# Kernel tuning notes

Measured on AMD Instinct MI355X. Metric: run time of the kernel, lower is better.

The kernel has to match this reference:

```python
import jax, jax.numpy as jnp
import numpy as np

A = 32      # num_agents (nodes per batch element)
B = 256     # batch size
T = 5       # temporal_window_size
H, C = 4, 64  # attention heads, hidden_dim per head
D = H * C   # feature_dim = 256
NEG_SLOPE = 0.2
LATENT = 128
NBS = 64    # num_belief_states
FIN = NBS + 16  # node_feat_dim = num_belief_states + action_dim


def _xavier(k, shape):
    std = (2.0 / (shape[0] + shape[-1])) ** 0.5
    return std * jax.random.normal(k, shape, dtype=jnp.float32)


def setup_inputs() -> dict:
    key = jax.random.key(0)
    ks = jax.random.split(key, 24)
    N = B * A
    # fully-connected directed graph (no self loops) inside each batch block
    ii, jj = np.meshgrid(np.arange(A), np.arange(A), indexing='ij')
    m = ii != jj
    off = (np.arange(B) * A)[:, None]
    src = (off + ii[m][None, :]).ravel()
    dst = (off + jj[m][None, :]).ravel()
    edge_index = jnp.asarray(np.stack([src, dst]), dtype=jnp.int32)  # [2, E]
    return dict(
        x_seq=jax.random.normal(ks[0], (T, N, FIN), dtype=jnp.float32),
        edge_index=edge_index,
        W1=_xavier(ks[1], (D, FIN)),
        att_src1=0.1 * jax.random.normal(ks[2], (H, C), dtype=jnp.float32),
        att_dst1=0.1 * jax.random.normal(ks[3], (H, C), dtype=jnp.float32),
        b1=jnp.zeros((D,), jnp.float32),
        W2=_xavier(ks[4], (D, D)),
        att_src2=0.1 * jax.random.normal(ks[5], (H, C), dtype=jnp.float32),
        att_dst2=0.1 * jax.random.normal(ks[6], (H, C), dtype=jnp.float32),
        b2=jnp.zeros((D,), jnp.float32),
        in_proj_w=_xavier(ks[7], (3 * D, D)),
        in_proj_b=jnp.zeros((3 * D,), jnp.float32),
        out_proj_w=_xavier(ks[8], (D, D)),
        out_proj_b=jnp.zeros((D,), jnp.float32),
        w_mean=_xavier(ks[9], (LATENT, D)),
        b_mean=jnp.zeros((LATENT,), jnp.float32),
        w_logvar=_xavier(ks[10], (LATENT, D)),
        b_logvar=jnp.zeros((LATENT,), jnp.float32),
        w_belief=_xavier(ks[11], (NBS, D)),
        b_belief=jnp.zeros((NBS,), jnp.float32),
    )


def _gat(x, src, dst, W, a_src, a_dst, bias, N):
    """PyG-style GATConv (concat heads, self loops already in src/dst, eval mode)."""
    h = (x @ W.T).reshape(N, H, C)                         # [N,H,C]
    e = (h * a_src).sum(-1)[src] + (h * a_dst).sum(-1)[dst]  # [E,H]
    e = jax.nn.leaky_relu(e, NEG_SLOPE)
    mx = jax.ops.segment_max(e, dst, num_segments=N)       # segment softmax over incoming edges
    ex = jnp.exp(e - mx[dst])
    denom = jax.ops.segment_sum(ex, dst, num_segments=N)
    alpha = ex / denom[dst]                                # [E,H]
    out = jax.ops.segment_sum(h[src] * alpha[:, :, None], dst, num_segments=N)
    return out.reshape(N, H * C) + bias


def reference(x_seq, edge_index, W1, att_src1, att_dst1, b1, W2, att_src2, att_dst2, b2,
              in_proj_w, in_proj_b, out_proj_w, out_proj_b,
              w_mean, b_mean, w_logvar, b_logvar, w_belief, b_belief):
    N = x_seq.shape[1]
    loops = jnp.arange(N, dtype=edge_index.dtype)          # GATConv adds self loops
    src = jnp.concatenate([edge_index[0], loops])
    dst = jnp.concatenate([edge_index[1], loops])
    ego = jnp.arange(0, N, A)                              # ego node of each batch element

    def step(_, x):
        hh = jax.nn.relu(_gat(x, src, dst, W1, att_src1, att_dst1, b1, N))
        hh = jax.nn.relu(_gat(hh, src, dst, W2, att_src2, att_dst2, b2, N))
        return None, hh[ego]                               # [B, D]

    _, outs = jax.lax.scan(step, None, x_seq)              # [T, B, D]
    seq = jnp.transpose(outs, (1, 0, 2))                   # [B, T, D]

    # nn.MultiheadAttention(batch_first=True), float additive mask of 1s (j<=i) / 0s (j>i)
    qkv = seq @ in_proj_w.T + in_proj_b
    q, k, v = jnp.split(qkv, 3, axis=-1)
    split = lambda t: t.reshape(B, T, H, D // H).transpose(0, 2, 1, 3)  # [B,H,T,dh]
    q, k, v = split(q), split(k), split(v)
    mask = (jnp.arange(T)[:, None] >= jnp.arange(T)[None, :]).astype(seq.dtype)
    scale = 1.0 / jnp.sqrt(jnp.asarray(D // H, seq.dtype))
    scores = jnp.einsum('bhqd,bhkd->bhqk', q, k) * scale + mask
    attn = jax.nn.softmax(scores, axis=-1)
    ctx = jnp.einsum('bhqk,bhkd->bhqd', attn, v).transpose(0, 2, 1, 3).reshape(B, T, D)
    attn_out = ctx @ out_proj_w.T + out_proj_b
    feat = attn_out[:, -1]                                 # [B, D]

    mean = feat @ w_mean.T + b_mean
    logvar = feat @ w_logvar.T + b_logvar
    belief = jax.nn.softmax(feat @ w_belief.T + b_belief, axis=-1)
    return mean, logvar, belief
```

## Files before the change

### kernel.cpp

```cpp
#include <hip/hip_runtime.h>

typedef _Float16 f16;
typedef __attribute__((ext_vector_type(2))) _Float16 f16x2;
typedef __attribute__((ext_vector_type(4))) _Float16 f16x4;
typedef __attribute__((ext_vector_type(8))) _Float16 f16x8;
typedef __attribute__((ext_vector_type(4))) float    f32x4;

#define NA 32
#define NB 256
#define NT 5
#define ND 256
#define NFIN 80
#define NLAT 128
#define NBEL 64
#define NEG 0.2f

#define W1K 96
#define XSTR 104
#define H1TSTR 40
#define HH1STR 264
#define ALSTR 40

#define OFF_XS  0
#define OFF_ALP 6656
#define OFF_HH1 0
#define OFF_H1T 16896
#define OFF_SD  37376
#define SMEM_SZ 38400

#define MFMA16(a,b,c) __builtin_amdgcn_mfma_f32_16x16x32_f16(a, b, c, 0, 0, 0)

#define WS_SEQ   0
#define WS_QKV   655360
#define WS_CTX   2621440
#define WS_W1F   2752512
#define WS_W2F   2801664
#define WS_IPW   2932736
#define WS_OPW   3325952
#define WS_HDW   3457024
#define WS_WSD1  3620864
#define WS_WSD2  3623936

__global__ void convert_w(const float* __restrict__ W1, const float* __restrict__ W2,
                          const float* __restrict__ ipw, const float* __restrict__ opw,
                          const float* __restrict__ wm, const float* __restrict__ wl,
                          const float* __restrict__ wb,
                          const float* __restrict__ as1, const float* __restrict__ ad1,
                          const float* __restrict__ as2, const float* __restrict__ ad2,
                          f16* __restrict__ W1f, f16* __restrict__ W2f,
                          f16* __restrict__ ipwf, f16* __restrict__ opwf,
                          f16* __restrict__ hdwf,
                          f16* __restrict__ wsd1f, f16* __restrict__ wsd2f)
{
    const int i = blockIdx.x * 256 + threadIdx.x;
    if (i < 24576) {
        const int r = i / W1K, c = i - r * W1K;
        W1f[i] = (c < NFIN) ? (f16)W1[r * NFIN + c] : (f16)0.f;
    } else if (i < 90112) {
        const int j = i - 24576; W2f[j] = (f16)W2[j];
    } else if (i < 286720) {
        const int j = i - 90112; ipwf[j] = (f16)ipw[j];
    } else if (i < 352256) {
        const int j = i - 286720; opwf[j] = (f16)opw[j];
    } else if (i < 434176) {
        const int j = i - 352256;
        hdwf[j] = (f16)(j < 32768 ? wm[j] : (j < 65536 ? wl[j - 32768] : wb[j - 65536]));
    } else if (i < 435712) {
        const int j = i - 434176;
        const int o = j / 96, f = j - o * 96;
        float v = 0.f;
        if (o < 8 && f < NFIN) {
            const int h = o & 3;
            const float* av = (o < 4) ? as1 : ad1;
            for (int cc = 0; cc < 64; ++cc)
                v = fmaf(av[h * 64 + cc], W1[(h * 64 + cc) * NFIN + f], v);
        }
        wsd1f[j] = (f16)v;
    } else if (i < 439808) {
        const int j = i - 435712;
        const int o = j >> 8, k = j & 255;
        float v = 0.f;
        if (o < 8) {
            const int h = o & 3;
            const float* av = (o < 4) ? as2 : ad2;
            for (int cc = 0; cc < 64; ++cc)
                v = fmaf(av[h * 64 + cc], W2[(h * 64 + cc) * ND + k], v);
        }
        wsd2f[j] = (f16)v;
    }
}

__global__ __launch_bounds__(256, 4)
void gnn_kernel(const float* __restrict__ x_seq,
                const f16*  __restrict__ W1f,  const f16* __restrict__ wsd1f,
                const float* __restrict__ b1,
                const f16*  __restrict__ W2f,  const f16* __restrict__ wsd2f,
                const float* __restrict__ b2,
                f16* __restrict__ seqf)
{
    __shared__ __align__(16) unsigned char smem[SMEM_SZ];
    f16*  Xs  = (f16*)(smem + OFF_XS);
    f16*  hh1 = (f16*)(smem + OFF_HH1);
    f16*  alp = (f16*)(smem + OFF_ALP);
    f16*  h1T = (f16*)(smem + OFF_H1T);
    float* sA = (float*)(smem + OFF_SD);
    float* dA = sA + 128;

    const int blk  = blockIdx.x;
    const int b    = blk / NT;
    const int t    = blk % NT;
    const int tid  = threadIdx.x;
    const int wv   = tid >> 6;
    const int lane = tid & 63;
    const int c    = lane & 15;
    const int g    = lane >> 4;
    const int n0   = wv * 64;

    const float* xg = x_seq + ((size_t)t * (NB * NA) + (size_t)b * NA) * NFIN;
    for (int idx = tid; idx < 640; idx += 256) {
        const int r = idx / 20, c4 = idx - r * 20;
        const float4 v = ((const float4*)xg)[idx];
        f16x4 h; h.x = (f16)v.x; h.y = (f16)v.y; h.z = (f16)v.z; h.w = (f16)v.w;
        *(f16x4*)(Xs + r * XSTR + c4 * 4) = h;
    }
    if (tid < 128) {
        const int r = tid >> 2, cc = tid & 3;
        f16x4 z; z.x = z.y = z.z = z.w = (f16)0.f;
        *(f16x4*)(Xs + r * XSTR + 80 + cc * 4) = z;
    }
    __syncthreads();

    f32x4 acc1[2][4]; f32x4 accS[2];
#pragma unroll
    for (int m = 0; m < 2; ++m) {
        accS[m] = (f32x4)0.f;
#pragma unroll
        for (int tn = 0; tn < 4; ++tn) acc1[m][tn] = (f32x4)0.f;
    }
#pragma unroll
    for (int kt = 0; kt < 3; ++kt) {
        const int k0 = kt * 32 + 8 * g;
        f16x8 a0 = *(const f16x8*)(Xs + c * XSTR + k0);
        f16x8 a1 = *(const f16x8*)(Xs + (16 + c) * XSTR + k0);
        f16x8 bs = *(const f16x8*)(wsd1f + c * W1K + k0);
        accS[0] = MFMA16(a0, bs, accS[0]);
        accS[1] = MFMA16(a1, bs, accS[1]);
#pragma unroll
        for (int tn = 0; tn < 4; ++tn) {
            f16x8 bw = *(const f16x8*)(W1f + (size_t)(n0 + 16 * tn + c) * W1K + k0);
            acc1[0][tn] = MFMA16(a0, bw, acc1[0][tn]);
            acc1[1][tn] = MFMA16(a1, bw, acc1[1][tn]);
        }
    }

    if (c == wv) {
#pragma unroll
        for (int m = 0; m < 2; ++m)
#pragma unroll
            for (int r = 0; r < 4; ++r)
                sA[wv * 32 + 16 * m + 4 * g + r] = accS[m][r];
    } else if (c == wv + 4) {
#pragma unroll
        for (int m = 0; m < 2; ++m)
#pragma unroll
            for (int r = 0; r < 4; ++r)
                dA[wv * 32 + 16 * m + 4 * g + r] = accS[m][r];
    }

#pragma unroll
    for (int m = 0; m < 2; ++m)
#pragma unroll
        for (int tn = 0; tn < 4; ++tn) {
            f16x4 h;
            h.x = (f16)acc1[m][tn][0]; h.y = (f16)acc1[m][tn][1];
            h.z = (f16)acc1[m][tn][2]; h.w = (f16)acc1[m][tn][3];
            *(f16x4*)(h1T + (n0 + 16 * tn + c) * H1TSTR + 16 * m + 4 * g) = h;
        }

    {
        const int j = lane & 31;
        const int half = lane >> 5;
        const float dd = dA[wv * 32 + j];
        const float* sbase = sA + wv * 32 + 16 * half;
        float e[16]; float mx = -1e30f;
#pragma unroll
        for (int i = 0; i < 16; ++i) {
            float v = sbase[i] + dd;
            v = (v >= 0.f) ? v : NEG * v;
            e[i] = v; mx = fmaxf(mx, v);
        }
        mx = fmaxf(mx, __shfl_xor(mx, 32, 64));
        float den = 0.f;
#pragma unroll
        for (int i = 0; i < 16; ++i) { float p = __expf(e[i] - mx); e[i] = p; den += p; }
        den += __shfl_xor(den, 32, 64);
        const float rr = 1.f / den;
        f16* arow = alp + (wv * 32 + j) * ALSTR + 16 * half;
#pragma unroll
        for (int i2 = 0; i2 < 8; ++i2) {
            f16x2 p2; p2.x = (f16)(e[2 * i2] * rr); p2.y = (f16)(e[2 * i2 + 1] * rr);
            *(f16x2*)(arow + 2 * i2) = p2;
        }
    }

    f32x4 agg[2][4];
#pragma unroll
    for (int m = 0; m < 2; ++m)
#pragma unroll
        for (int tn = 0; tn < 4; ++tn) agg[m][tn] = (f32x4)0.f;
    {
        f16x8 aal0 = *(const f16x8*)(alp + (wv * 32 + c) * ALSTR + 8 * g);
        f16x8 aal1 = *(const f16x8*)(alp + (wv * 32 + 16 + c) * ALSTR + 8 * g);
#pragma unroll
        for (int tn = 0; tn < 4; ++tn) {
            f16x8 bh = *(const f16x8*)(h1T + (n0 + 16 * tn + c) * H1TSTR + 8 * g);
            agg[0][tn] = MFMA16(aal0, bh, agg[0][tn]);
            agg[1][tn] = MFMA16(aal1, bh, agg[1][tn]);
        }
    }

    __syncthreads();

    {
        float b1v[4];
#pragma unroll
        for (int tn = 0; tn < 4; ++tn) b1v[tn] = b1[n0 + 16 * tn + c];
#pragma unroll
        for (int m = 0; m < 2; ++m)
#pragma unroll
            for (int tn = 0; tn < 4; ++tn)
#pragma unroll
                for (int r = 0; r < 4; ++r) {
                    float val = fmaxf(agg[m][tn][r] + b1v[tn], 0.f);
                    hh1[(16 * m + 4 * g + r) * HH1STR + n0 + 16 * tn + c] = (f16)val;
                }
    }
    __syncthreads();

    f32x4 acc2[2][4]; f32x4 accS2[2];
#pragma unroll
    for (int m = 0; m < 2; ++m) {
        accS2[m] = (f32x4)0.f;
#pragma unroll
        for (int tn = 0; tn < 4; ++tn) acc2[m][tn] = (f32x4)0.f;
    }
#pragma unroll
    for (int kt = 0; kt < 8; ++kt) {
        const int k0 = kt * 32 + 8 * g;
        f16x8 a0 = *(const f16x8*)(hh1 + c * HH1STR + k0);
        f16x8 a1 = *(const f16x8*)(hh1 + (16 + c) * HH1STR + k0);
        f16x8 bs = *(const f16x8*)(wsd2f + c * ND + k0);
        accS2[0] = MFMA16(a0, bs, accS2[0]);
        accS2[1] = MFMA16(a1, bs, accS2[1]);
#pragma unroll
        for (int tn = 0; tn < 4; ++tn) {
            f16x8 bw = *(const f16x8*)(W2f + (size_t)(n0 + 16 * tn + c) * ND + k0);
            acc2[0][tn] = MFMA16(a0, bw, acc2[0][tn]);
            acc2[1][tn] = MFMA16(a1, bw, acc2[1][tn]);
        }
    }

    if (c == wv) {
#pragma unroll
        for (int m = 0; m < 2; ++m)
#pragma unroll
            for (int r = 0; r < 4; ++r)
                sA[wv * 32 + 16 * m + 4 * g + r] = accS2[m][r];
    }
    if (c == wv + 4 && g == 0) dA[wv * 32] = accS2[0][0];

    const float d20 = dA[wv * 32];

    {
        float mx = -1e30f;
#pragma unroll
        for (int i = 0; i < 32; ++i) {
            float v = sA[wv * 32 + i] + d20;
            v = (v >= 0.f) ? v : NEG * v;
            mx = fmaxf(mx, v);
        }
        float den = 0.f;
#pragma unroll
        for (int i = 0; i < 32; ++i) {
            float v = sA[wv * 32 + i] + d20;
            v = (v >= 0.f) ? v : NEG * v;
            den += __expf(v - mx);
        }
        float ev[2][4];
#pragma unroll
        for (int m = 0; m < 2; ++m)
#pragma unroll
            for (int r = 0; r < 4; ++r) {
                float v = sA[wv * 32 + 16 * m + 4 * g + r] + d20;
                v = (v >= 0.f) ? v : NEG * v;
                ev[m][r] = __expf(v - mx);
            }
        float b2v[4];
#pragma unroll
        for (int tn = 0; tn < 4; ++tn) b2v[tn] = b2[n0 + 16 * tn + c];
        const float rden = 1.f / den;
        f16* sq = seqf + ((size_t)b * NT + t) * ND;
#pragma unroll
        for (int tn = 0; tn < 4; ++tn) {
            float o = 0.f;
#pragma unroll
            for (int m = 0; m < 2; ++m)
#pragma unroll
                for (int r = 0; r < 4; ++r) o = fmaf(ev[m][r], acc2[m][tn][r], o);
            o += __shfl_xor(o, 16, 64);
            o += __shfl_xor(o, 32, 64);
            if (g == 0) sq[n0 + 16 * tn + c] = (f16)fmaxf(o * rden + b2v[tn], 0.f);
        }
    }
}

#define QASTR 264
__global__ __launch_bounds__(256, 4)
void qkv_kernel(const f16* __restrict__ seqf, const f16* __restrict__ ipwf,
                const float* __restrict__ ipb, f16* __restrict__ qkv)
{
    __shared__ __align__(16) f16 As[64 * QASTR];

    const int bx  = blockIdx.x;
    const int m0  = (bx % 20) * 64;
    const int n0  = (bx / 20) * 128;
    const int tid = threadIdx.x;
    const int wv  = tid >> 6;
    const int lane = tid & 63;
    const int c   = lane & 15;
    const int g   = lane >> 4;
    const int mb  = (wv >> 1) * 32;
    const int nb  = n0 + (wv & 1) * 64;

    for (int idx = tid; idx < 2048; idx += 256) {
        const int r = idx >> 5, c8 = idx & 31;
        *(f16x8*)(As + r * QASTR + c8 * 8) =
            *(const f16x8*)(seqf + (size_t)(m0 + r) * ND + c8 * 8);
    }
    __syncthreads();

    f32x4 acc[2][4];
#pragma unroll
    for (int m = 0; m < 2; ++m)
#pragma unroll
        for (int tn = 0; tn < 4; ++tn) acc[m][tn] = (f32x4)0.f;

#pragma unroll
    for (int kt = 0; kt < 8; ++kt) {
        const int k0 = kt * 32 + 8 * g;
        f16x8 a0 = *(const f16x8*)(As + (mb + c) * QASTR + k0);
        f16x8 a1 = *(const f16x8*)(As + (mb + 16 + c) * QASTR + k0);
#pragma unroll
        for (int tn = 0; tn < 4; ++tn) {
            f16x8 bw = *(const f16x8*)(ipwf + (size_t)(nb + 16 * tn + c) * ND + k0);
            acc[0][tn] = MFMA16(a0, bw, acc[0][tn]);
            acc[1][tn] = MFMA16(a1, bw, acc[1][tn]);
        }
    }

    float bias[4];
#pragma unroll
    for (int tn = 0; tn < 4; ++tn) bias[tn] = ipb[nb + 16 * tn + c];
#pragma unroll
    for (int m = 0; m < 2; ++m)
#pragma unroll
        for (int tn = 0; tn < 4; ++tn)
#pragma unroll
            for (int r = 0; r < 4; ++r) {
                const int row = m0 + mb + 16 * m + 4 * g + r;
                qkv[(size_t)row * 768 + nb + 16 * tn + c] =
                    (f16)(acc[m][tn][r] + bias[tn]);
            }
}

__global__ __launch_bounds__(256, 4)
void attn_kernel(const f16* __restrict__ qkv, f16* __restrict__ ctx)
{
    const int b    = blockIdx.x;
    const int wv   = threadIdx.x >> 6;
    const int lane = threadIdx.x & 63;
    const int ch   = wv * 64 + lane;

    const float q = (float)qkv[(size_t)(b * 5 + 4) * 768 + ch];
    float kv[NT], vv[NT];
#pragma unroll
    for (int t = 0; t < NT; ++t) {
        kv[t] = (float)qkv[(size_t)(b * 5 + t) * 768 + 256 + ch];
        vv[t] = (float)qkv[(size_t)(b * 5 + t) * 768 + 512 + ch];
    }
    float sc[NT];
#pragma unroll
    for (int t = 0; t < NT; ++t) {
        float p = q * kv[t];
#pragma unroll
        for (int off = 32; off > 0; off >>= 1) p += __shfl_xor(p, off, 64);
        sc[t] = p * 0.125f;
    }
    float m = sc[0];
#pragma unroll
    for (int t = 1; t < NT; ++t) m = fmaxf(m, sc[t]);
    float den = 0.f, o = 0.f;
#pragma unroll
    for (int t = 0; t < NT; ++t) {
        float p = __expf(sc[t] - m);
        den += p;
        o = fmaf(p, vv[t], o);
    }
    ctx[(size_t)b * ND + ch] = (f16)(o / den);
}

#define FASTR 264
__global__ __launch_bounds__(256, 2)
void final_kernel(const f16* __restrict__ ctx,
                  const f16* __restrict__ opwf, const float* __restrict__ opb,
                  const f16* __restrict__ hdwf,
                  const float* __restrict__ bm, const float* __restrict__ blv,
                  const float* __restrict__ bb,
                  float* __restrict__ out)
{
    __shared__ __align__(16) f16 As[32 * FASTR];
    __shared__ __align__(16) f16 Fs[32 * FASTR];
    __shared__ __align__(16) float Bs[32 * 68];

    const int m0   = blockIdx.x * 32;
    const int tid  = threadIdx.x;
    const int wv   = tid >> 6;
    const int lane = tid & 63;
    const int c    = lane & 15;
    const int g    = lane >> 4;

    for (int idx = tid; idx < 1024; idx += 256) {
        const int r = idx >> 5, c8 = idx & 31;
        *(f16x8*)(As + r * FASTR + c8 * 8) =
            *(const f16x8*)(ctx + (size_t)(m0 + r) * ND + c8 * 8);
    }
    __syncthreads();

    {
        f32x4 acc[2][4];
#pragma unroll
        for (int m = 0; m < 2; ++m)
#pragma unroll
            for (int tn = 0; tn < 4; ++tn) acc[m][tn] = (f32x4)0.f;
#pragma unroll
        for (int kt = 0; kt < 8; ++kt) {
            const int k0 = kt * 32 + 8 * g;
            f16x8 a0 = *(const f16x8*)(As + c * FASTR + k0);
            f16x8 a1 = *(const f16x8*)(As + (16 + c) * FASTR + k0);
#pragma unroll
            for (int tn = 0; tn < 4; ++tn) {
                f16x8 bw = *(const f16x8*)(opwf + (size_t)(wv * 64 + 16 * tn + c) * ND + k0);
                acc[0][tn] = MFMA16(a0, bw, acc[0][tn]);
                acc[1][tn] = MFMA16(a1, bw, acc[1][tn]);
            }
        }
        float bias[4];
#pragma unroll
        for (int tn = 0; tn < 4; ++tn) bias[tn] = opb[wv * 64 + 16 * tn + c];
#pragma unroll
        for (int m = 0; m < 2; ++m)
#pragma unroll
            for (int tn = 0; tn < 4; ++tn)
#pragma unroll
                for (int r = 0; r < 4; ++r)
                    Fs[(16 * m + 4 * g + r) * FASTR + wv * 64 + 16 * tn + c] =
                        (f16)(acc[m][tn][r] + bias[tn]);
    }
    __syncthreads();

    {
        f32x4 acc[2][5];
#pragma unroll
        for (int m = 0; m < 2; ++m)
#pragma unroll
            for (int fi = 0; fi < 5; ++fi) acc[m][fi] = (f32x4)0.f;
#pragma unroll
        for (int kt = 0; kt < 8; ++kt) {
            const int k0 = kt * 32 + 8 * g;
            f16x8 a0 = *(const f16x8*)(Fs + c * FASTR + k0);
            f16x8 a1 = *(const f16x8*)(Fs + (16 + c) * FASTR + k0);
#pragma unroll
            for (int fi = 0; fi < 5; ++fi) {
                const int nf = 5 * wv + fi;
                f16x8 bw = *(const f16x8*)(hdwf + (size_t)(16 * nf + c) * ND + k0);
                acc[0][fi] = MFMA16(a0, bw, acc[0][fi]);
                acc[1][fi] = MFMA16(a1, bw, acc[1][fi]);
            }
        }
#pragma unroll
        for (int fi = 0; fi < 5; ++fi) {
            const int ocol = 16 * (5 * wv + fi) + c;
            float bias;
            if (ocol < 128)       bias = bm[ocol];
            else if (ocol < 256)  bias = blv[ocol - 128];
            else                  bias = bb[ocol - 256];
#pragma unroll
            for (int m = 0; m < 2; ++m)
#pragma unroll
                for (int r = 0; r < 4; ++r) {
                    const int row = 16 * m + 4 * g + r;
                    const float v = acc[m][fi][r] + bias;
                    if (ocol < 128)
                        out[(size_t)(m0 + row) * NLAT + ocol] = v;
                    else if (ocol < 256)
                        out[(size_t)NB * NLAT + (size_t)(m0 + row) * NLAT + (ocol - 128)] = v;
                    else
                        Bs[row * 68 + (ocol - 256)] = v;
                }
        }
    }
    __syncthreads();

    for (int rr = 0; rr < 8; ++rr) {
        const int row = wv * 8 + rr;
        float x = Bs[row * 68 + lane];
        float mm = x;
#pragma unroll
        for (int off = 32; off > 0; off >>= 1) mm = fmaxf(mm, __shfl_xor(mm, off, 64));
        float p = __expf(x - mm);
        float dd = p;
#pragma unroll
        for (int off = 32; off > 0; off >>= 1) dd += __shfl_xor(dd, off, 64);
        out[(size_t)2 * NB * NLAT + (size_t)(m0 + row) * NBEL + lane] = p / dd;
    }
}

extern "C" void kernel_launch(void* const* d_in, const int* in_sizes, int n_in,
                              void* d_out, int out_size, void* d_ws, size_t ws_size,
                              hipStream_t stream)
{
    (void)in_sizes; (void)n_in; (void)out_size; (void)ws_size;
    const float* x_seq = (const float*)d_in[0];
    const float* W1  = (const float*)d_in[2];
    const float* as1 = (const float*)d_in[3];
    const float* ad1 = (const float*)d_in[4];
    const float* b1  = (const float*)d_in[5];
    const float* W2  = (const float*)d_in[6];
    const float* as2 = (const float*)d_in[7];
    const float* ad2 = (const float*)d_in[8];
    const float* b2  = (const float*)d_in[9];
    const float* ipw = (const float*)d_in[10];
    const float* ipb = (const float*)d_in[11];
    const float* opw = (const float*)d_in[12];
    const float* opb = (const float*)d_in[13];
    const float* wm  = (const float*)d_in[14];
    const float* bm  = (const float*)d_in[15];
    const float* wl  = (const float*)d_in[16];
    const float* bl  = (const float*)d_in[17];
    const float* wb  = (const float*)d_in[18];
    const float* bb  = (const float*)d_in[19];

    char* ws = (char*)d_ws;
    f16* seqf  = (f16*)(ws + WS_SEQ);
    f16* qkv   = (f16*)(ws + WS_QKV);
    f16* ctx   = (f16*)(ws + WS_CTX);
    f16* W1f   = (f16*)(ws + WS_W1F);
    f16* W2f   = (f16*)(ws + WS_W2F);
    f16* ipwf  = (f16*)(ws + WS_IPW);
    f16* opwf  = (f16*)(ws + WS_OPW);
    f16* hdwf  = (f16*)(ws + WS_HDW);
    f16* wsd1f = (f16*)(ws + WS_WSD1);
    f16* wsd2f = (f16*)(ws + WS_WSD2);
    float* out = (float*)d_out;

    hipLaunchKernelGGL(convert_w, dim3(1718), dim3(256), 0, stream,
                       W1, W2, ipw, opw, wm, wl, wb, as1, ad1, as2, ad2,
                       W1f, W2f, ipwf, opwf, hdwf, wsd1f, wsd2f);
    hipLaunchKernelGGL(gnn_kernel, dim3(NB * NT), dim3(256), 0, stream,
                       x_seq, W1f, wsd1f, b1, W2f, wsd2f, b2, seqf);
    hipLaunchKernelGGL(qkv_kernel, dim3(120), dim3(256), 0, stream,
                       seqf, ipwf, ipb, qkv);
    hipLaunchKernelGGL(attn_kernel, dim3(NB), dim3(256), 0, stream, qkv, ctx);
    hipLaunchKernelGGL(final_kernel, dim3(8), dim3(256), 0, stream,
                       ctx, opwf, opb, hdwf, bm, bl, bb, out);
}
```

Measured before the change: 71.33 us.

## Software-prefetch global weight fragments in MFMA loops and transpose aggregation output

The GEMM k-loops in the GNN and QKV kernels now double-buffer their global weight fragments in registers, loading the next k-slice before issuing the MFMAs on the current one. This hides global/L2 latency behind MFMA work. The attention-aggregation MFMA swaps its operands to produce a transposed tile, so the bias+ReLU writeback can use vectorized float4 bias loads and f16x4 shared-memory stores. Launch bounds drop from 4 to 3 blocks per CU to leave room for the extra live registers, which may reduce occupancy.

```diff
diff --git a/kernel.cpp b/kernel.cpp
--- a/kernel.cpp
+++ b/kernel.cpp
@@ -90,7 +90,7 @@
     }
 }
 
-__global__ __launch_bounds__(256, 4)
+__global__ __launch_bounds__(256, 3)
 void gnn_kernel(const float* __restrict__ x_seq,
                 const f16*  __restrict__ W1f,  const f16* __restrict__ wsd1f,
                 const float* __restrict__ b1,
@@ -137,19 +137,35 @@
 #pragma unroll
         for (int tn = 0; tn < 4; ++tn) acc1[m][tn] = (f32x4)0.f;
     }
-#pragma unroll
-    for (int kt = 0; kt < 3; ++kt) {
-        const int k0 = kt * 32 + 8 * g;
-        f16x8 a0 = *(const f16x8*)(Xs + c * XSTR + k0);
-        f16x8 a1 = *(const f16x8*)(Xs + (16 + c) * XSTR + k0);
-        f16x8 bs = *(const f16x8*)(wsd1f + c * W1K + k0);
-        accS[0] = MFMA16(a0, bs, accS[0]);
-        accS[1] = MFMA16(a1, bs, accS[1]);
-#pragma unroll
-        for (int tn = 0; tn < 4; ++tn) {
-            f16x8 bw = *(const f16x8*)(W1f + (size_t)(n0 + 16 * tn + c) * W1K + k0);
-            acc1[0][tn] = MFMA16(a0, bw, acc1[0][tn]);
-            acc1[1][tn] = MFMA16(a1, bw, acc1[1][tn]);
+    {
+        const int kg = 8 * g;
+        f16x8 bs = *(const f16x8*)(wsd1f + c * W1K + kg);
+        f16x8 bw0 = *(const f16x8*)(W1f + (size_t)(n0 + c) * W1K + kg);
+        f16x8 bw1 = *(const f16x8*)(W1f + (size_t)(n0 + 16 + c) * W1K + kg);
+        f16x8 bw2 = *(const f16x8*)(W1f + (size_t)(n0 + 32 + c) * W1K + kg);
+        f16x8 bw3 = *(const f16x8*)(W1f + (size_t)(n0 + 48 + c) * W1K + kg);
+#pragma unroll
+        for (int kt = 0; kt < 3; ++kt) {
+            const int k0 = kt * 32 + kg;
+            const int kn = (kt < 2 ? k0 + 32 : k0);
+            f16x8 nbs  = *(const f16x8*)(wsd1f + c * W1K + kn);
+            f16x8 nbw0 = *(const f16x8*)(W1f + (size_t)(n0 + c) * W1K + kn);
+            f16x8 nbw1 = *(const f16x8*)(W1f + (size_t)(n0 + 16 + c) * W1K + kn);
+            f16x8 nbw2 = *(const f16x8*)(W1f + (size_t)(n0 + 32 + c) * W1K + kn);
+            f16x8 nbw3 = *(const f16x8*)(W1f + (size_t)(n0 + 48 + c) * W1K + kn);
+            f16x8 a0 = *(const f16x8*)(Xs + c * XSTR + k0);
+            f16x8 a1 = *(const f16x8*)(Xs + (16 + c) * XSTR + k0);
+            accS[0] = MFMA16(a0, bs, accS[0]);
+            accS[1] = MFMA16(a1, bs, accS[1]);
+            acc1[0][0] = MFMA16(a0, bw0, acc1[0][0]);
+            acc1[1][0] = MFMA16(a1, bw0, acc1[1][0]);
+            acc1[0][1] = MFMA16(a0, bw1, acc1[0][1]);
+            acc1[1][1] = MFMA16(a1, bw1, acc1[1][1]);
+            acc1[0][2] = MFMA16(a0, bw2, acc1[0][2]);
+            acc1[1][2] = MFMA16(a1, bw2, acc1[1][2]);
+            acc1[0][3] = MFMA16(a0, bw3, acc1[0][3]);
+            acc1[1][3] = MFMA16(a1, bw3, acc1[1][3]);
+            bs = nbs; bw0 = nbw0; bw1 = nbw1; bw2 = nbw2; bw3 = nbw3;
         }
     }
 
@@ -203,37 +219,38 @@
         }
     }
 
-    f32x4 agg[2][4];
-#pragma unroll
-    for (int m = 0; m < 2; ++m)
-#pragma unroll
-        for (int tn = 0; tn < 4; ++tn) agg[m][tn] = (f32x4)0.f;
-    {
-        f16x8 aal0 = *(const f16x8*)(alp + (wv * 32 + c) * ALSTR + 8 * g);
-        f16x8 aal1 = *(const f16x8*)(alp + (wv * 32 + 16 + c) * ALSTR + 8 * g);
-#pragma unroll
-        for (int tn = 0; tn < 4; ++tn) {
-            f16x8 bh = *(const f16x8*)(h1T + (n0 + 16 * tn + c) * H1TSTR + 8 * g);
-            agg[0][tn] = MFMA16(aal0, bh, agg[0][tn]);
-            agg[1][tn] = MFMA16(aal1, bh, agg[1][tn]);
+    f32x4 accT[4][2];
+#pragma unroll
+    for (int mt = 0; mt < 4; ++mt)
+#pragma unroll
+        for (int jt = 0; jt < 2; ++jt) accT[mt][jt] = (f32x4)0.f;
+    {
+        f16x8 bal0 = *(const f16x8*)(alp + (wv * 32 + c) * ALSTR + 8 * g);
+        f16x8 bal1 = *(const f16x8*)(alp + (wv * 32 + 16 + c) * ALSTR + 8 * g);
+#pragma unroll
+        for (int mt = 0; mt < 4; ++mt) {
+            f16x8 ah = *(const f16x8*)(h1T + (n0 + 16 * mt + c) * H1TSTR + 8 * g);
+            accT[mt][0] = MFMA16(ah, bal0, accT[mt][0]);
+            accT[mt][1] = MFMA16(ah, bal1, accT[mt][1]);
         }
     }
 
     __syncthreads();
 
     {
-        float b1v[4];
-#pragma unroll
-        for (int tn = 0; tn < 4; ++tn) b1v[tn] = b1[n0 + 16 * tn + c];
-#pragma unroll
-        for (int m = 0; m < 2; ++m)
-#pragma unroll
-            for (int tn = 0; tn < 4; ++tn)
-#pragma unroll
-                for (int r = 0; r < 4; ++r) {
-                    float val = fmaxf(agg[m][tn][r] + b1v[tn], 0.f);
-                    hh1[(16 * m + 4 * g + r) * HH1STR + n0 + 16 * tn + c] = (f16)val;
-                }
+#pragma unroll
+        for (int mt = 0; mt < 4; ++mt) {
+            const float4 bq = *(const float4*)&b1[n0 + 16 * mt + 4 * g];
+#pragma unroll
+            for (int jt = 0; jt < 2; ++jt) {
+                f16x4 h;
+                h.x = (f16)fmaxf(accT[mt][jt][0] + bq.x, 0.f);
+                h.y = (f16)fmaxf(accT[mt][jt][1] + bq.y, 0.f);
+                h.z = (f16)fmaxf(accT[mt][jt][2] + bq.z, 0.f);
+                h.w = (f16)fmaxf(accT[mt][jt][3] + bq.w, 0.f);
+                *(f16x4*)(hh1 + (16 * jt + c) * HH1STR + n0 + 16 * mt + 4 * g) = h;
+            }
+        }
     }
     __syncthreads();
 
@@ -244,19 +261,35 @@
 #pragma unroll
         for (int tn = 0; tn < 4; ++tn) acc2[m][tn] = (f32x4)0.f;
     }
-#pragma unroll
-    for (int kt = 0; kt < 8; ++kt) {
-        const int k0 = kt * 32 + 8 * g;
-        f16x8 a0 = *(const f16x8*)(hh1 + c * HH1STR + k0);
-        f16x8 a1 = *(const f16x8*)(hh1 + (16 + c) * HH1STR + k0);
-        f16x8 bs = *(const f16x8*)(wsd2f + c * ND + k0);
-        accS2[0] = MFMA16(a0, bs, accS2[0]);
-        accS2[1] = MFMA16(a1, bs, accS2[1]);
-#pragma unroll
-        for (int tn = 0; tn < 4; ++tn) {
-            f16x8 bw = *(const f16x8*)(W2f + (size_t)(n0 + 16 * tn + c) * ND + k0);
-            acc2[0][tn] = MFMA16(a0, bw, acc2[0][tn]);
-            acc2[1][tn] = MFMA16(a1, bw, acc2[1][tn]);
+    {
+        const int kg = 8 * g;
+        f16x8 bs = *(const f16x8*)(wsd2f + c * ND + kg);
+        f16x8 bw0 = *(const f16x8*)(W2f + (size_t)(n0 + c) * ND + kg);
+        f16x8 bw1 = *(const f16x8*)(W2f + (size_t)(n0 + 16 + c) * ND + kg);
+        f16x8 bw2 = *(const f16x8*)(W2f + (size_t)(n0 + 32 + c) * ND + kg);
+        f16x8 bw3 = *(const f16x8*)(W2f + (size_t)(n0 + 48 + c) * ND + kg);
+#pragma unroll
+        for (int kt = 0; kt < 8; ++kt) {
+            const int k0 = kt * 32 + kg;
+            const int kn = (kt < 7 ? k0 + 32 : k0);
+            f16x8 nbs  = *(const f16x8*)(wsd2f + c * ND + kn);
+            f16x8 nbw0 = *(const f16x8*)(W2f + (size_t)(n0 + c) * ND + kn);
+            f16x8 nbw1 = *(const f16x8*)(W2f + (size_t)(n0 + 16 + c) * ND + kn);
+            f16x8 nbw2 = *(const f16x8*)(W2f + (size_t)(n0 + 32 + c) * ND + kn);
+            f16x8 nbw3 = *(const f16x8*)(W2f + (size_t)(n0 + 48 + c) * ND + kn);
+            f16x8 a0 = *(const f16x8*)(hh1 + c * HH1STR + k0);
+            f16x8 a1 = *(const f16x8*)(hh1 + (16 + c) * HH1STR + k0);
+            accS2[0] = MFMA16(a0, bs, accS2[0]);
+            accS2[1] = MFMA16(a1, bs, accS2[1]);
+            acc2[0][0] = MFMA16(a0, bw0, acc2[0][0]);
+            acc2[1][0] = MFMA16(a1, bw0, acc2[1][0]);
+            acc2[0][1] = MFMA16(a0, bw1, acc2[0][1]);
+            acc2[1][1] = MFMA16(a1, bw1, acc2[1][1]);
+            acc2[0][2] = MFMA16(a0, bw2, acc2[0][2]);
+            acc2[1][2] = MFMA16(a1, bw2, acc2[1][2]);
+            acc2[0][3] = MFMA16(a0, bw3, acc2[0][3]);
+            acc2[1][3] = MFMA16(a1, bw3, acc2[1][3]);
+            bs = nbs; bw0 = nbw0; bw1 = nbw1; bw2 = nbw2; bw3 = nbw3;
         }
     }
 
@@ -345,16 +378,31 @@
 #pragma unroll
         for (int tn = 0; tn < 4; ++tn) acc[m][tn] = (f32x4)0.f;
 
-#pragma unroll
-    for (int kt = 0; kt < 8; ++kt) {
-        const int k0 = kt * 32 + 8 * g;
-        f16x8 a0 = *(const f16x8*)(As + (mb + c) * QASTR + k0);
-        f16x8 a1 = *(const f16x8*)(As + (mb + 16 + c) * QASTR + k0);
-#pragma unroll
-        for (int tn = 0; tn < 4; ++tn) {
-            f16x8 bw = *(const f16x8*)(ipwf + (size_t)(nb + 16 * tn + c) * ND + k0);
-            acc[0][tn] = MFMA16(a0, bw, acc[0][tn]);
-            acc[1][tn] = MFMA16(a1, bw, acc[1][tn]);
+    {
+        const int kg = 8 * g;
+        f16x8 bw0 = *(const f16x8*)(ipwf + (size_t)(nb + c) * ND + kg);
+        f16x8 bw1 = *(const f16x8*)(ipwf + (size_t)(nb + 16 + c) * ND + kg);
+        f16x8 bw2 = *(const f16x8*)(ipwf + (size_t)(nb + 32 + c) * ND + kg);
+        f16x8 bw3 = *(const f16x8*)(ipwf + (size_t)(nb + 48 + c) * ND + kg);
+#pragma unroll
+        for (int kt = 0; kt < 8; ++kt) {
+            const int k0 = kt * 32 + kg;
+            const int kn = (kt < 7 ? k0 + 32 : k0);
+            f16x8 nbw0 = *(const f16x8*)(ipwf + (size_t)(nb + c) * ND + kn);
+            f16x8 nbw1 = *(const f16x8*)(ipwf + (size_t)(nb + 16 + c) * ND + kn);
+            f16x8 nbw2 = *(const f16x8*)(ipwf + (size_t)(nb + 32 + c) * ND + kn);
+            f16x8 nbw3 = *(const f16x8*)(ipwf + (size_t)(nb + 48 + c) * ND + kn);
+            f16x8 a0 = *(const f16x8*)(As + (mb + c) * QASTR + k0);
+            f16x8 a1 = *(const f16x8*)(As + (mb + 16 + c) * QASTR + k0);
+            acc[0][0] = MFMA16(a0, bw0, acc[0][0]);
+            acc[1][0] = MFMA16(a1, bw0, acc[1][0]);
+            acc[0][1] = MFMA16(a0, bw1, acc[0][1]);
+            acc[1][1] = MFMA16(a1, bw1, acc[1][1]);
+            acc[0][2] = MFMA16(a0, bw2, acc[0][2]);
+            acc[1][2] = MFMA16(a1, bw2, acc[1][2]);
+            acc[0][3] = MFMA16(a0, bw3, acc[0][3]);
+            acc[1][3] = MFMA16(a1, bw3, acc[1][3]);
+            bw0 = nbw0; bw1 = nbw1; bw2 = nbw2; bw3 = nbw3;
         }
     }
 
```

After: 71.38 us. About the same (+0.1%).

## Reassociate second GAT layer: aggregate ego features before W2 projection

Applied to the files above, without the earlier changes.

Only the ego node's output of the second GAT layer is needed, so the kernel now forms the attention-weighted sum of layer-1 features (z = sum_j alpha_j h1_j) before the W2 projection rather than projecting all 32 nodes. That projection moves into a new batched seq_kernel GEMM over all (b,t) rows, removing the per-block 32x256x256 W2 MFMA work. It also transposes the layer-1 aggregation MFMA to allow vectorised stores, preloads W1 and attention-weight fragments into registers before the x load, and lowers launch bounds to 2 waves per SIMD. The cost is an extra kernel launch and a workspace round-trip for z, which reuses the qkv buffer region.

```diff
diff --git a/kernel.cpp b/kernel.cpp
--- a/kernel.cpp
+++ b/kernel.cpp
@@ -32,6 +32,7 @@
 
 #define WS_SEQ   0
 #define WS_QKV   655360
+#define WS_Z2    655360
 #define WS_CTX   2621440
 #define WS_W1F   2752512
 #define WS_W2F   2801664
@@ -90,13 +91,12 @@
     }
 }
 
-__global__ __launch_bounds__(256, 4)
+__global__ __launch_bounds__(256, 2)
 void gnn_kernel(const float* __restrict__ x_seq,
                 const f16*  __restrict__ W1f,  const f16* __restrict__ wsd1f,
                 const float* __restrict__ b1,
-                const f16*  __restrict__ W2f,  const f16* __restrict__ wsd2f,
-                const float* __restrict__ b2,
-                f16* __restrict__ seqf)
+                const f16*  __restrict__ wsd2f,
+                f16* __restrict__ z2g)
 {
     __shared__ __align__(16) unsigned char smem[SMEM_SZ];
     f16*  Xs  = (f16*)(smem + OFF_XS);
@@ -115,6 +115,17 @@
     const int c    = lane & 15;
     const int g    = lane >> 4;
     const int n0   = wv * 64;
+    const int kg   = 8 * g;
+
+    f16x8 w1s[3], w1b[3][4];
+#pragma unroll
+    for (int kt = 0; kt < 3; ++kt) {
+        const int k0 = kt * 32 + kg;
+        w1s[kt] = *(const f16x8*)(wsd1f + c * W1K + k0);
+#pragma unroll
+        for (int tn = 0; tn < 4; ++tn)
+            w1b[kt][tn] = *(const f16x8*)(W1f + (size_t)(n0 + 16 * tn + c) * W1K + k0);
+    }
 
     const float* xg = x_seq + ((size_t)t * (NB * NA) + (size_t)b * NA) * NFIN;
     for (int idx = tid; idx < 640; idx += 256) {
@@ -139,17 +150,15 @@
     }
 #pragma unroll
     for (int kt = 0; kt < 3; ++kt) {
-        const int k0 = kt * 32 + 8 * g;
+        const int k0 = kt * 32 + kg;
         f16x8 a0 = *(const f16x8*)(Xs + c * XSTR + k0);
         f16x8 a1 = *(const f16x8*)(Xs + (16 + c) * XSTR + k0);
-        f16x8 bs = *(const f16x8*)(wsd1f + c * W1K + k0);
-        accS[0] = MFMA16(a0, bs, accS[0]);
-        accS[1] = MFMA16(a1, bs, accS[1]);
+        accS[0] = MFMA16(a0, w1s[kt], accS[0]);
+        accS[1] = MFMA16(a1, w1s[kt], accS[1]);
 #pragma unroll
         for (int tn = 0; tn < 4; ++tn) {
-            f16x8 bw = *(const f16x8*)(W1f + (size_t)(n0 + 16 * tn + c) * W1K + k0);
-            acc1[0][tn] = MFMA16(a0, bw, acc1[0][tn]);
-            acc1[1][tn] = MFMA16(a1, bw, acc1[1][tn]);
+            acc1[0][tn] = MFMA16(a0, w1b[kt][tn], acc1[0][tn]);
+            acc1[1][tn] = MFMA16(a1, w1b[kt][tn], acc1[1][tn]);
         }
     }
 
@@ -203,61 +212,56 @@
         }
     }
 
-    f32x4 agg[2][4];
-#pragma unroll
-    for (int m = 0; m < 2; ++m)
-#pragma unroll
-        for (int tn = 0; tn < 4; ++tn) agg[m][tn] = (f32x4)0.f;
+    f32x4 accT[4][2];
+#pragma unroll
+    for (int mt = 0; mt < 4; ++mt)
+#pragma unroll
+        for (int jt = 0; jt < 2; ++jt) accT[mt][jt] = (f32x4)0.f;
     {
-        f16x8 aal0 = *(const f16x8*)(alp + (wv * 32 + c) * ALSTR + 8 * g);
-        f16x8 aal1 = *(const f16x8*)(alp + (wv * 32 + 16 + c) * ALSTR + 8 * g);
-#pragma unroll
-        for (int tn = 0; tn < 4; ++tn) {
-            f16x8 bh = *(const f16x8*)(h1T + (n0 + 16 * tn + c) * H1TSTR + 8 * g);
-            agg[0][tn] = MFMA16(aal0, bh, agg[0][tn]);
-            agg[1][tn] = MFMA16(aal1, bh, agg[1][tn]);
-        }
-    }
-
-    __syncthreads();
-
-    {
-        float b1v[4];
-#pragma unroll
-        for (int tn = 0; tn < 4; ++tn) b1v[tn] = b1[n0 + 16 * tn + c];
-#pragma unroll
-        for (int m = 0; m < 2; ++m)
-#pragma unroll
-            for (int tn = 0; tn < 4; ++tn)
-#pragma unroll
-                for (int r = 0; r < 4; ++r) {
-                    float val = fmaxf(agg[m][tn][r] + b1v[tn], 0.f);
-                    hh1[(16 * m + 4 * g + r) * HH1STR + n0 + 16 * tn + c] = (f16)val;
-                }
-    }
-    __syncthreads();
-
-    f32x4 acc2[2][4]; f32x4 accS2[2];
-#pragma unroll
-    for (int m = 0; m < 2; ++m) {
-        accS2[m] = (f32x4)0.f;
-#pragma unroll
-        for (int tn = 0; tn < 4; ++tn) acc2[m][tn] = (f32x4)0.f;
-    }
+        f16x8 bal0 = *(const f16x8*)(alp + (wv * 32 + c) * ALSTR + kg);
+        f16x8 bal1 = *(const f16x8*)(alp + (wv * 32 + 16 + c) * ALSTR + kg);
+#pragma unroll
+        for (int mt = 0; mt < 4; ++mt) {
+            f16x8 ah = *(const f16x8*)(h1T + (n0 + 16 * mt + c) * H1TSTR + kg);
+            accT[mt][0] = MFMA16(ah, bal0, accT[mt][0]);
+            accT[mt][1] = MFMA16(ah, bal1, accT[mt][1]);
+        }
+    }
+
+    __syncthreads();
+
+    f32x4 bqa[4];
+#pragma unroll
+    for (int mt = 0; mt < 4; ++mt)
+        bqa[mt] = *(const f32x4*)&b1[n0 + 16 * mt + 4 * g];
+#pragma unroll
+    for (int mt = 0; mt < 4; ++mt) {
+#pragma unroll
+        for (int jt = 0; jt < 2; ++jt) {
+            f16x4 h;
+            h.x = (f16)fmaxf(accT[mt][jt][0] + bqa[mt][0], 0.f);
+            h.y = (f16)fmaxf(accT[mt][jt][1] + bqa[mt][1], 0.f);
+            h.z = (f16)fmaxf(accT[mt][jt][2] + bqa[mt][2], 0.f);
+            h.w = (f16)fmaxf(accT[mt][jt][3] + bqa[mt][3], 0.f);
+            *(f16x4*)(hh1 + (16 * jt + c) * HH1STR + n0 + 16 * mt + 4 * g) = h;
+        }
+    }
+    __syncthreads();
+
+    f16x8 w2s[8];
+#pragma unroll
+    for (int kt = 0; kt < 8; ++kt)
+        w2s[kt] = *(const f16x8*)(wsd2f + c * ND + kt * 32 + kg);
+
+    f32x4 accS2[2];
+    accS2[0] = (f32x4)0.f; accS2[1] = (f32x4)0.f;
 #pragma unroll
     for (int kt = 0; kt < 8; ++kt) {
-        const int k0 = kt * 32 + 8 * g;
+        const int k0 = kt * 32 + kg;
         f16x8 a0 = *(const f16x8*)(hh1 + c * HH1STR + k0);
         f16x8 a1 = *(const f16x8*)(hh1 + (16 + c) * HH1STR + k0);
-        f16x8 bs = *(const f16x8*)(wsd2f + c * ND + k0);
-        accS2[0] = MFMA16(a0, bs, accS2[0]);
-        accS2[1] = MFMA16(a1, bs, accS2[1]);
-#pragma unroll
-        for (int tn = 0; tn < 4; ++tn) {
-            f16x8 bw = *(const f16x8*)(W2f + (size_t)(n0 + 16 * tn + c) * ND + k0);
-            acc2[0][tn] = MFMA16(a0, bw, acc2[0][tn]);
-            acc2[1][tn] = MFMA16(a1, bw, acc2[1][tn]);
-        }
+        accS2[0] = MFMA16(a0, w2s[kt], accS2[0]);
+        accS2[1] = MFMA16(a1, w2s[kt], accS2[1]);
     }
 
     if (c == wv) {
@@ -286,35 +290,104 @@
             v = (v >= 0.f) ? v : NEG * v;
             den += __expf(v - mx);
         }
-        float ev[2][4];
-#pragma unroll
-        for (int m = 0; m < 2; ++m)
+        float e0, e1;
+        {
+            float v = sA[wv * 32 + c] + d20;
+            v = (v >= 0.f) ? v : NEG * v;
+            e0 = __expf(v - mx);
+        }
+        {
+            float v = sA[wv * 32 + 16 + c] + d20;
+            v = (v >= 0.f) ? v : NEG * v;
+            e1 = __expf(v - mx);
+        }
+        const float rden = 1.f / den;
+        f16* zo = z2g + (size_t)blk * ND;
+#pragma unroll
+        for (int mt = 0; mt < 4; ++mt) {
+            f32x4 zv;
 #pragma unroll
             for (int r = 0; r < 4; ++r) {
-                float v = sA[wv * 32 + 16 * m + 4 * g + r] + d20;
-                v = (v >= 0.f) ? v : NEG * v;
-                ev[m][r] = __expf(v - mx);
+                const float h0 = fmaxf(accT[mt][0][r] + bqa[mt][r], 0.f);
+                const float h1v = fmaxf(accT[mt][1][r] + bqa[mt][r], 0.f);
+                zv[r] = e0 * h0 + e1 * h1v;
             }
-        float b2v[4];
-#pragma unroll
-        for (int tn = 0; tn < 4; ++tn) b2v[tn] = b2[n0 + 16 * tn + c];
-        const float rden = 1.f / den;
-        f16* sq = seqf + ((size_t)b * NT + t) * ND;
+#pragma unroll
+            for (int r = 0; r < 4; ++r) {
+                zv[r] += __shfl_xor(zv[r], 1, 64);
+                zv[r] += __shfl_xor(zv[r], 2, 64);
+                zv[r] += __shfl_xor(zv[r], 4, 64);
+                zv[r] += __shfl_xor(zv[r], 8, 64);
+            }
+            if (c == 0) {
+                f16x4 h;
+                h.x = (f16)(zv[0] * rden); h.y = (f16)(zv[1] * rden);
+                h.z = (f16)(zv[2] * rden); h.w = (f16)(zv[3] * rden);
+                *(f16x4*)(zo + n0 + 16 * mt + 4 * g) = h;
+            }
+        }
+    }
+}
+
+#define QASTR 264
+__global__ __launch_bounds__(256, 4)
+void seq_kernel(const f16* __restrict__ z2g, const f16* __restrict__ W2f,
+                const float* __restrict__ b2, f16* __restrict__ seqf)
+{
+    __shared__ __align__(16) f16 As[64 * QASTR];
+
+    const int bx  = blockIdx.x;
+    const int m0  = (bx % 20) * 64;
+    const int n0  = (bx / 20) * 128;
+    const int tid = threadIdx.x;
+    const int wv  = tid >> 6;
+    const int lane = tid & 63;
+    const int c   = lane & 15;
+    const int g   = lane >> 4;
+    const int mb  = (wv >> 1) * 32;
+    const int nb  = n0 + (wv & 1) * 64;
+
+    for (int idx = tid; idx < 2048; idx += 256) {
+        const int r = idx >> 5, c8 = idx & 31;
+        *(f16x8*)(As + r * QASTR + c8 * 8) =
+            *(const f16x8*)(z2g + (size_t)(m0 + r) * ND + c8 * 8);
+    }
+    __syncthreads();
+
+    f32x4 acc[2][4];
+#pragma unroll
+    for (int m = 0; m < 2; ++m)
+#pragma unroll
+        for (int tn = 0; tn < 4; ++tn) acc[m][tn] = (f32x4)0.f;
+
+#pragma unroll
+    for (int kt = 0; kt < 8; ++kt) {
+        const int k0 = kt * 32 + 8 * g;
+        f16x8 a0 = *(const f16x8*)(As + (mb + c) * QASTR + k0);
+        f16x8 a1 = *(const f16x8*)(As + (mb + 16 + c) * QASTR + k0);
 #pragma unroll
         for (int tn = 0; tn < 4; ++tn) {
-            float o = 0.f;
-#pragma unroll
-            for (int m = 0; m < 2; ++m)
-#pragma unroll
-                for (int r = 0; r < 4; ++r) o = fmaf(ev[m][r], acc2[m][tn][r], o);
-            o += __shfl_xor(o, 16, 64);
-            o += __shfl_xor(o, 32, 64);
-            if (g == 0) sq[n0 + 16 * tn + c] = (f16)fmaxf(o * rden + b2v[tn], 0.f);
-        }
-    }
+            f16x8 bw = *(const f16x8*)(W2f + (size_t)(nb + 16 * tn + c) * ND + k0);
+            acc[0][tn] = MFMA16(a0, bw, acc[0][tn]);
+            acc[1][tn] = MFMA16(a1, bw, acc[1][tn]);
+        }
+    }
+
+    float bias[4];
+#pragma unroll
+    for (int tn = 0; tn < 4; ++tn) bias[tn] = b2[nb + 16 * tn + c];
+#pragma unroll
+    for (int m = 0; m < 2; ++m)
+#pragma unroll
+        for (int tn = 0; tn < 4; ++tn)
+#pragma unroll
+            for (int r = 0; r < 4; ++r) {
+                const int row = m0 + mb + 16 * m + 4 * g + r;
+                seqf[(size_t)row * ND + nb + 16 * tn + c] =
+                    (f16)fmaxf(acc[m][tn][r] + bias[tn], 0.f);
+            }
 }
 
-#define QASTR 264
 __global__ __launch_bounds__(256, 4)
 void qkv_kernel(const f16* __restrict__ seqf, const f16* __restrict__ ipwf,
                 const float* __restrict__ ipb, f16* __restrict__ qkv)
@@ -553,6 +626,7 @@
     char* ws = (char*)d_ws;
     f16* seqf  = (f16*)(ws + WS_SEQ);
     f16* qkv   = (f16*)(ws + WS_QKV);
+    f16* z2g   = (f16*)(ws + WS_Z2);
     f16* ctx   = (f16*)(ws + WS_CTX);
     f16* W1f   = (f16*)(ws + WS_W1F);
     f16* W2f   = (f16*)(ws + WS_W2F);
@@ -567,7 +641,9 @@
                        W1, W2, ipw, opw, wm, wl, wb, as1, ad1, as2, ad2,
                        W1f, W2f, ipwf, opwf, hdwf, wsd1f, wsd2f);
     hipLaunchKernelGGL(gnn_kernel, dim3(NB * NT), dim3(256), 0, stream,
-                       x_seq, W1f, wsd1f, b1, W2f, wsd2f, b2, seqf);
+                       x_seq, W1f, wsd1f, b1, wsd2f, z2g);
+    hipLaunchKernelGGL(seq_kernel, dim3(40), dim3(256), 0, stream,
+                       z2g, W2f, b2, seqf);
     hipLaunchKernelGGL(qkv_kernel, dim3(120), dim3(256), 0, stream,
                        seqf, ipwf, ipb, qkv);
     hipLaunchKernelGGL(attn_kernel, dim3(NB), dim3(256), 0, stream, qkv, ctx);
```

New measurement: 62.16 us, median of 4. 12.9% less time.
